# Performance work log

Measured on AMD Instinct MI355X. Metric: run time of the kernel, lower is better.

## Reference

```python
import jax, jax.numpy as jnp
import numpy as np

STALK_DIM = 16
N_NODES = 50000
N_EDGES = 400000
HIDDEN = 64


def setup_inputs() -> dict:
    key = jax.random.key(0)
    k1, k2, k3, k4 = jax.random.split(key, 4)
    d = STALK_DIM
    x = jax.random.normal(k1, (N_NODES, d), dtype=jnp.float32)
    edge_index = jax.random.randint(k2, (2, N_EDGES), 0, N_NODES, dtype=jnp.int64)
    W1 = jax.random.normal(k3, (HIDDEN, 2 * d), dtype=jnp.float32) * (1.0 / np.sqrt(2 * d))
    b1 = jnp.zeros((HIDDEN,), dtype=jnp.float32)
    W2 = jax.random.normal(k4, (d, HIDDEN), dtype=jnp.float32) * (1.0 / np.sqrt(HIDDEN))
    b2 = jnp.zeros((d,), dtype=jnp.float32)
    return {"x": x, "edge_index": edge_index, "W1": W1, "b1": b1, "W2": W2, "b2": b2}


def reference(x, edge_index, W1, b1, W2, b2):
    d = x.shape[1]
    n = x.shape[0]
    src, dst = edge_index[0], edge_index[1]
    xs, xd = x[src], x[dst]  # [E, d]

    def reflection(a, b):
        h = jax.nn.relu(jnp.concatenate([a, b], axis=1) @ W1.T + b1)
        return h @ W2.T + b2  # [E, d]

    def householder(v):
        # F.normalize(v, dim=1): v / max(||v||, 1e-12)
        vn = v / jnp.maximum(jnp.linalg.norm(v, axis=1, keepdims=True), 1e-12)
        return jnp.eye(d, dtype=v.dtype)[None] - 2.0 * vn[:, :, None] * vn[:, None, :]

    F_s = householder(reflection(xs, xd))  # [E, d, d]
    F_d = householder(reflection(xd, xs))  # [E, d, d]
    L_sd = -jnp.einsum('eki,ekj->eij', F_s, F_d)  # -F_s^T @ F_d, [E, d, d]

    # degrees: both endpoints of every edge contribute 1
    ones_e = jnp.ones(src.shape[0], dtype=x.dtype)
    deg = jnp.zeros(n, dtype=x.dtype).at[src].add(ones_e).at[dst].add(ones_e)
    deg_inv_sqrt = 1.0 / jnp.sqrt(jnp.maximum(deg, 1e-5))
    # D_inv_sqrt is scalar*I per node, so normalization is a scalar coefficient per edge
    coef = deg_inv_sqrt[src] * deg_inv_sqrt[dst]  # [E]

    # out[s] -= D^-1/2_s L D^-1/2_d x[d] ; out[d] -= D^-1/2_d L^T D^-1/2_s x[s]
    msg_s = coef[:, None] * jnp.einsum('eij,ej->ei', L_sd, xd)  # goes to src
    msg_d = coef[:, None] * jnp.einsum('eji,ej->ei', L_sd, xs)  # goes to dst

    out = x - jnp.zeros_like(x).at[src].add(msg_s) - jnp.zeros_like(x).at[dst].add(msg_d)
    return jax.nn.relu(out)
```

## Files before the change

kernel.cpp:

```cpp
#include <hip/hip_runtime.h>
#include <hip/hip_bf16.h>
#include <hip/hip_fp16.h>

#define N_NODES 50000
#define N_EDGES 400000
#define D 16
#define HID 64

#define SCAN_B 256
#define SCAN_G ((N_NODES + SCAN_B - 1) / SCAN_B)

typedef unsigned short ushort_t;
typedef _Float16 h16x2 __attribute__((ext_vector_type(2)));

#define CNT4_OFF  0
#define DEG_OFF   (4 * N_NODES)
#define OFF_OFF   (5 * N_NODES)
#define CUR_OFF   (6 * N_NODES + 1)
#define BS_OFF    (7 * N_NODES + 1)
#define MSG_OFF_I (((BS_OFF + SCAN_G) + 3) & ~3)
#define PREP_OFF  (MSG_OFF_I + 2 * N_EDGES * D)
#define PREP_DW   (32 * 52 + 16)
#define CSR_NEEDED_BYTES ((size_t)(PREP_OFF + PREP_DW) * 4 + 64)

#define FB_NDEG   (N_NODES)
#define FB_NACC   (N_NODES * D)
#define FB_FLAGS  (FB_NDEG + FB_NACC)

__device__ __forceinline__ float bf_bits(ushort_t us) {
    return __uint_as_float(((unsigned)us) << 16);
}
__device__ __forceinline__ float lo_bf(unsigned u) { return __uint_as_float(u << 16); }
__device__ __forceinline__ float hi_bf(unsigned u) { return __uint_as_float(u & 0xffff0000u); }
__device__ __forceinline__ ushort_t f2bf(float v) {
    unsigned u = __float_as_uint(v);
    unsigned r = (u + 0x7fffu + ((u >> 16) & 1u)) >> 16;
    return (ushort_t)r;
}
__device__ __forceinline__ float ld_f(const void* p, int idx, int f32) {
    return f32 ? ((const float*)p)[idx]
               : bf_bits(((const ushort_t*)p)[idx]);
}

__device__ __forceinline__ unsigned pack_h2(float a, float b) {
#if __has_builtin(__builtin_amdgcn_cvt_pkrtz)
    return __builtin_bit_cast(unsigned, __builtin_amdgcn_cvt_pkrtz(a, b));
#else
    h16x2 h;
    h.x = (_Float16)a;
    h.y = (_Float16)b;
    return __builtin_bit_cast(unsigned, h);
#endif
}

#if __has_builtin(__builtin_amdgcn_fdot2)
__device__ __forceinline__ float fdot2u(unsigned a, unsigned b, float c) {
    return __builtin_amdgcn_fdot2(__builtin_bit_cast(h16x2, a),
                                  __builtin_bit_cast(h16x2, b), c, false);
}
#else
__device__ __forceinline__ float fdot2u(unsigned a, unsigned b, float c) {
    h16x2 ha = __builtin_bit_cast(h16x2, a);
    h16x2 hb = __builtin_bit_cast(h16x2, b);
    return fmaf((float)ha.x, (float)hb.x, fmaf((float)ha.y, (float)hb.y, c));
}
#endif

__device__ __forceinline__ void load16(const void* __restrict__ p, long long base,
                                       int f32, float* o) {
    if (f32) {
        const float4* q = (const float4*)((const float*)p + base);
        float4 a = q[0], b = q[1], c = q[2], d = q[3];
        o[0]=a.x; o[1]=a.y; o[2]=a.z; o[3]=a.w;
        o[4]=b.x; o[5]=b.y; o[6]=b.z; o[7]=b.w;
        o[8]=c.x; o[9]=c.y; o[10]=c.z; o[11]=c.w;
        o[12]=d.x; o[13]=d.y; o[14]=d.z; o[15]=d.w;
    } else {
        const uint4* q = (const uint4*)((const ushort_t*)p + base);
        uint4 a = q[0], b = q[1];
        unsigned u[8] = {a.x, a.y, a.z, a.w, b.x, b.y, b.z, b.w};
#pragma unroll
        for (int k = 0; k < 8; k++) {
            o[2 * k]     = lo_bf(u[k]);
            o[2 * k + 1] = hi_bf(u[k]);
        }
    }
}

__device__ __forceinline__ void load_edge(const void* __restrict__ ei, int e, int is64,
                                          int& s, int& d) {
    if (is64) {
        const long long* p = (const long long*)ei;
        s = (int)p[e];
        d = (int)p[N_EDGES + e];
    } else {
        const int* p = (const int*)ei;
        s = p[e];
        d = p[N_EDGES + e];
    }
}

__device__ __forceinline__ void detect_flags(const void* x, const void* ei, int* flags) {
    const ushort_t* h = (const ushort_t*)x;
    int f32 = 0;
    for (int k = 0; k < 256; k++) {
        float v = bf_bits(h[k]);
        if (!(v == v) || fabsf(v) > 1.0e6f) { f32 = 1; break; }
    }
    const long long* p = (const long long*)ei;
    int i64 = 1;
    for (int k = 0; k < 16; k++) {
        long long v = p[k];
        if (v < 0 || v >= N_NODES) { i64 = 0; break; }
    }
    flags[0] = f32;
    flags[1] = i64;
}

__device__ __forceinline__ void stage_weights(
    const void* W1, const void* b1, const void* W2, const void* b2, int f32,
    float* sW1, float* sW2t, float* sb1, float* sb2)
{
    int t = threadIdx.x;
    for (int idx = t; idx < HID * 2 * D; idx += blockDim.x)
        sW1[idx] = ld_f(W1, idx, f32);
    for (int idx = t; idx < HID * D; idx += blockDim.x) {
        int j = idx / D, i = idx % D;
        sW2t[idx] = ld_f(W2, i * HID + j, f32);
    }
    if (t < HID) sb1[t] = ld_f(b1, t, f32);
    if (t < D)  sb2[t] = ld_f(b2, t, f32);
}

__device__ __forceinline__ void edge_math_v4(
    const float* __restrict__ sW1, const float* __restrict__ sW2t,
    const float* __restrict__ sb1, const float* __restrict__ sb2,
    const float* xs, const float* xd, float coef,
    float* ms, float* md)
{
    float vs[D], vd[D];
#pragma unroll
    for (int i = 0; i < D; i++) { vs[i] = sb2[i]; vd[i] = sb2[i]; }
#pragma unroll 4
    for (int j = 0; j < HID; j++) {
        float hs = sb1[j], hd = sb1[j];
        const float4* w4 = (const float4*)&sW1[j * 2 * D];
#pragma unroll
        for (int t = 0; t < 4; t++) {
            float4 wv = w4[t];
            int k = 4 * t;
            hs = fmaf(wv.x, xs[k],     hs); hd = fmaf(wv.x, xd[k],     hd);
            hs = fmaf(wv.y, xs[k + 1], hs); hd = fmaf(wv.y, xd[k + 1], hd);
            hs = fmaf(wv.z, xs[k + 2], hs); hd = fmaf(wv.z, xd[k + 2], hd);
            hs = fmaf(wv.w, xs[k + 3], hs); hd = fmaf(wv.w, xd[k + 3], hd);
        }
#pragma unroll
        for (int t = 0; t < 4; t++) {
            float4 wv = w4[4 + t];
            int k = 4 * t;
            hs = fmaf(wv.x, xd[k],     hs); hd = fmaf(wv.x, xs[k],     hd);
            hs = fmaf(wv.y, xd[k + 1], hs); hd = fmaf(wv.y, xs[k + 1], hd);
            hs = fmaf(wv.z, xd[k + 2], hs); hd = fmaf(wv.z, xs[k + 2], hd);
            hs = fmaf(wv.w, xd[k + 3], hs); hd = fmaf(wv.w, xs[k + 3], hd);
        }
        hs = fmaxf(hs, 0.0f);
        hd = fmaxf(hd, 0.0f);
        const float4* w24 = (const float4*)&sW2t[j * D];
#pragma unroll
        for (int t = 0; t < 4; t++) {
            float4 u = w24[t];
            int i = 4 * t;
            vs[i]     = fmaf(u.x, hs, vs[i]);     vd[i]     = fmaf(u.x, hd, vd[i]);
            vs[i + 1] = fmaf(u.y, hs, vs[i + 1]); vd[i + 1] = fmaf(u.y, hd, vd[i + 1]);
            vs[i + 2] = fmaf(u.z, hs, vs[i + 2]); vd[i + 2] = fmaf(u.z, hd, vd[i + 2]);
            vs[i + 3] = fmaf(u.w, hs, vs[i + 3]); vd[i + 3] = fmaf(u.w, hd, vd[i + 3]);
        }
    }
    float ns = 0.0f, nd = 0.0f;
#pragma unroll
    for (int i = 0; i < D; i++) { ns = fmaf(vs[i], vs[i], ns); nd = fmaf(vd[i], vd[i], nd); }
    float is_ = 1.0f / fmaxf(sqrtf(ns), 1e-12f);
    float id_ = 1.0f / fmaxf(sqrtf(nd), 1e-12f);
#pragma unroll
    for (int i = 0; i < D; i++) { vs[i] *= is_; vd[i] *= id_; }
    float dot1 = 0.0f;
#pragma unroll
    for (int i = 0; i < D; i++) dot1 = fmaf(vd[i], xd[i], dot1);
#pragma unroll
    for (int i = 0; i < D; i++) ms[i] = fmaf(-2.0f * dot1, vd[i], xd[i]);
    float dot2 = 0.0f;
#pragma unroll
    for (int i = 0; i < D; i++) dot2 = fmaf(vs[i], ms[i], dot2);
#pragma unroll
    for (int i = 0; i < D; i++) ms[i] = coef * fmaf(-2.0f * dot2, vs[i], ms[i]);
    float dot3 = 0.0f;
#pragma unroll
    for (int i = 0; i < D; i++) dot3 = fmaf(vs[i], xs[i], dot3);
#pragma unroll
    for (int i = 0; i < D; i++) md[i] = fmaf(-2.0f * dot3, vs[i], xs[i]);
    float dot4 = 0.0f;
#pragma unroll
    for (int i = 0; i < D; i++) dot4 = fmaf(vd[i], md[i], dot4);
#pragma unroll
    for (int i = 0; i < D; i++) md[i] = coef * fmaf(-2.0f * dot4, vd[i], md[i]);
}

__global__ void csr_count_kernel(const void* __restrict__ ei,
                                 const void* __restrict__ x,
                                 const void* __restrict__ W1,
                                 const void* __restrict__ b1,
                                 const void* __restrict__ W2,
                                 const void* __restrict__ b2,
                                 int* __restrict__ wsI) {
    __shared__ int sfl[2];
    if (threadIdx.x == 0) detect_flags(x, ei, sfl);
    __syncthreads();
    int i64 = sfl[1];

    if (blockIdx.x == 0) {
        unsigned* pp = (unsigned*)(wsI + PREP_OFF);
        const ushort_t* W1b = (const ushort_t*)W1;
        const ushort_t* W2b = (const ushort_t*)W2;
        const ushort_t* b1b = (const ushort_t*)b1;
        const ushort_t* b2b = (const ushort_t*)b2;
        for (int idx = threadIdx.x; idx < 32 * 52; idx += 256) {
            int jj = idx / 52, w = idx % 52;
            unsigned val = 0;
            if (w < 32) {
                int row = 2 * jj + (w >> 4), k2 = w & 15;
                val = pack_h2(bf_bits(W1b[row * 32 + 2 * k2]),
                              bf_bits(W1b[row * 32 + 2 * k2 + 1]));
            } else if (w < 48) {
                int i = w - 32;
                val = pack_h2(bf_bits(W2b[i * HID + 2 * jj]),
                              bf_bits(W2b[i * HID + 2 * jj + 1]));
            } else if (w == 48) {
                val = __float_as_uint(bf_bits(b1b[2 * jj]));
            } else if (w == 49) {
                val = __float_as_uint(bf_bits(b1b[2 * jj + 1]));
            }
            pp[idx] = val;
        }
        if (threadIdx.x < D)
            pp[32 * 52 + threadIdx.x] = __float_as_uint(bf_bits(b2b[threadIdx.x]));
    }

    int e = blockIdx.x * blockDim.x + threadIdx.x;
    if (e >= N_EDGES) return;
    int s, d;
    load_edge(ei, e, i64, s, d);
    int r = (e & 3) * N_NODES;
    atomicAdd(&wsI[CNT4_OFF + r + s], 1);
    atomicAdd(&wsI[CNT4_OFF + r + d], 1);
}

__global__ __launch_bounds__(SCAN_B) void csr_scan1_kernel(int* __restrict__ wsI) {
    __shared__ int sm[SCAN_B];
    int t = threadIdx.x;
    int g = blockIdx.x * SCAN_B + t;
    int c = 0;
    if (g < N_NODES) {
        c = wsI[CNT4_OFF + g] + wsI[CNT4_OFF + N_NODES + g]
          + wsI[CNT4_OFF + 2 * N_NODES + g] + wsI[CNT4_OFF + 3 * N_NODES + g];
        wsI[DEG_OFF + g] = c;
    }
    sm[t] = c;
    __syncthreads();
    for (int st = SCAN_B / 2; st > 0; st >>= 1) {
        if (t < st) sm[t] += sm[t + st];
        __syncthreads();
    }
    if (t == 0) wsI[BS_OFF + blockIdx.x] = sm[0];
}

__global__ __launch_bounds__(SCAN_B) void csr_scan3_kernel(int* __restrict__ wsI) {
    __shared__ int sB[SCAN_B];
    __shared__ int sm[SCAN_B];
    int t = threadIdx.x;
    int bsv = (t < SCAN_G) ? wsI[BS_OFF + t] : 0;
    sB[t] = bsv;
    __syncthreads();
    for (int st = 1; st < SCAN_B; st <<= 1) {
        int u = (t >= st) ? sB[t - st] : 0;
        __syncthreads();
        sB[t] += u;
        __syncthreads();
    }
    int blockBase = sB[blockIdx.x] - wsI[BS_OFF + blockIdx.x];

    int g = blockIdx.x * SCAN_B + t;
    int c = (g < N_NODES) ? wsI[DEG_OFF + g] : 0;
    sm[t] = c;
    __syncthreads();
    for (int st = 1; st < SCAN_B; st <<= 1) {
        int u = (t >= st) ? sm[t - st] : 0;
        __syncthreads();
        sm[t] += u;
        __syncthreads();
    }
    int excl = sm[t] - c + blockBase;
    if (g < N_NODES) {
        wsI[OFF_OFF + g] = excl;
        wsI[CUR_OFF + g] = excl;
        if (g == N_NODES - 1) wsI[OFF_OFF + N_NODES] = excl + c;
    }
}

__global__ __launch_bounds__(256) void csr_edge_kernel(
    const void* __restrict__ x,
    const void* __restrict__ ei,
    const void* __restrict__ W1,
    const void* __restrict__ b1,
    const void* __restrict__ W2,
    const void* __restrict__ b2,
    const unsigned* __restrict__ prep,
    int* __restrict__ wsI)
{
    __shared__ __align__(16) float sW1f[HID * 2 * D];
    __shared__ __align__(16) float sW2tf[HID * D];
    __shared__ float sb1[HID];
    __shared__ float sb2[D];
    __shared__ int sfl[2];

    if (threadIdx.x == 0) detect_flags(x, ei, sfl);
    __syncthreads();
    int f32 = sfl[0], i64 = sfl[1];
    int t = threadIdx.x;

    if (f32) {
        for (int idx = t; idx < HID * 2 * D; idx += 256)
            sW1f[idx] = ld_f(W1, idx, 1);
        for (int idx = t; idx < HID * D; idx += 256) {
            int j = idx / D, i = idx % D;
            sW2tf[idx] = ld_f(W2, i * HID + j, 1);
        }
        if (t < HID) sb1[t] = ld_f(b1, t, 1);
        if (t < D)  sb2[t] = ld_f(b2, t, 1);
        __syncthreads();
    }

    int e = blockIdx.x * 256 + t;
    if (e >= N_EDGES) return;

    int s, d;
    load_edge(ei, e, i64, s, d);
    float degs = (float)wsI[DEG_OFF + s];
    float degd = (float)wsI[DEG_OFF + d];
    float coef = (1.0f / sqrtf(fmaxf(degs, 1e-5f))) * (1.0f / sqrtf(fmaxf(degd, 1e-5f)));
    float* msg = (float*)(wsI + MSG_OFF_I);

    if (!f32) {
        unsigned xsh[8], xdh[8];
        {
            const uint4* q = (const uint4*)((const ushort_t*)x + (long long)s * D);
            uint4 a = q[0], b = q[1];
            unsigned u[8] = {a.x, a.y, a.z, a.w, b.x, b.y, b.z, b.w};
#pragma unroll
            for (int k = 0; k < 8; k++) xsh[k] = pack_h2(lo_bf(u[k]), hi_bf(u[k]));
        }
        {
            const uint4* q = (const uint4*)((const ushort_t*)x + (long long)d * D);
            uint4 a = q[0], b = q[1];
            unsigned u[8] = {a.x, a.y, a.z, a.w, b.x, b.y, b.z, b.w};
#pragma unroll
            for (int k = 0; k < 8; k++) xdh[k] = pack_h2(lo_bf(u[k]), hi_bf(u[k]));
        }

        const float* b2f = (const float*)(prep + 32 * 52);
        float vs[D], vd[D];
#pragma unroll
        for (int i = 0; i < D; i++) { vs[i] = b2f[i]; vd[i] = b2f[i]; }

#pragma unroll 1
        for (int jj = 0; jj < 32; jj++) {
            const uint4* wb = (const uint4*)(prep + jj * 52);
            uint4 q0 = wb[0], q1 = wb[1], q2 = wb[2], q3 = wb[3];
            uint4 q4 = wb[4], q5 = wb[5], q6 = wb[6], q7 = wb[7];
            uint4 q8 = wb[8], q9 = wb[9], qA = wb[10], qB = wb[11];
            const float* bb = (const float*)(prep + jj * 52 + 48);
            float hs0 = bb[0], hd0 = bb[0];
            float hs1 = bb[1], hd1 = bb[1];

            unsigned r0[16] = {q0.x, q0.y, q0.z, q0.w, q1.x, q1.y, q1.z, q1.w,
                               q2.x, q2.y, q2.z, q2.w, q3.x, q3.y, q3.z, q3.w};
            unsigned r1[16] = {q4.x, q4.y, q4.z, q4.w, q5.x, q5.y, q5.z, q5.w,
                               q6.x, q6.y, q6.z, q6.w, q7.x, q7.y, q7.z, q7.w};
            unsigned w2a[16] = {q8.x, q8.y, q8.z, q8.w, q9.x, q9.y, q9.z, q9.w,
                                qA.x, qA.y, qA.z, qA.w, qB.x, qB.y, qB.z, qB.w};
#pragma unroll
            for (int k = 0; k < 8; k++) {
                hs0 = fdot2u(r0[k], xsh[k], hs0);
                hd0 = fdot2u(r0[k], xdh[k], hd0);
                hs1 = fdot2u(r1[k], xsh[k], hs1);
                hd1 = fdot2u(r1[k], xdh[k], hd1);
            }
#pragma unroll
            for (int k = 0; k < 8; k++) {
                hs0 = fdot2u(r0[8 + k], xdh[k], hs0);
                hd0 = fdot2u(r0[8 + k], xsh[k], hd0);
                hs1 = fdot2u(r1[8 + k], xdh[k], hs1);
                hd1 = fdot2u(r1[8 + k], xsh[k], hd1);
            }
            hs0 = fmaxf(hs0, 0.0f); hd0 = fmaxf(hd0, 0.0f);
            hs1 = fmaxf(hs1, 0.0f); hd1 = fmaxf(hd1, 0.0f);
            unsigned hsp = pack_h2(hs0, hs1);
            unsigned hdp = pack_h2(hd0, hd1);
#pragma unroll
            for (int i = 0; i < D; i++) {
                vs[i] = fdot2u(w2a[i], hsp, vs[i]);
                vd[i] = fdot2u(w2a[i], hdp, vd[i]);
            }
        }

        float xs[D], xd[D];
#pragma unroll
        for (int k = 0; k < 8; k++) {
            h16x2 a = __builtin_bit_cast(h16x2, xsh[k]);
            xs[2 * k] = (float)a.x; xs[2 * k + 1] = (float)a.y;
            h16x2 b = __builtin_bit_cast(h16x2, xdh[k]);
            xd[2 * k] = (float)b.x; xd[2 * k + 1] = (float)b.y;
        }

        float ns = 0.0f, nd = 0.0f;
#pragma unroll
        for (int i = 0; i < D; i++) { ns = fmaf(vs[i], vs[i], ns); nd = fmaf(vd[i], vd[i], nd); }
        float is_ = 1.0f / fmaxf(sqrtf(ns), 1e-12f);
        float id_ = 1.0f / fmaxf(sqrtf(nd), 1e-12f);
#pragma unroll
        for (int i = 0; i < D; i++) { vs[i] *= is_; vd[i] *= id_; }

        float ms[D], md[D];
        float dot1 = 0.0f;
#pragma unroll
        for (int i = 0; i < D; i++) dot1 = fmaf(vd[i], xd[i], dot1);
#pragma unroll
        for (int i = 0; i < D; i++) ms[i] = fmaf(-2.0f * dot1, vd[i], xd[i]);
        float dot2 = 0.0f;
#pragma unroll
        for (int i = 0; i < D; i++) dot2 = fmaf(vs[i], ms[i], dot2);
#pragma unroll
        for (int i = 0; i < D; i++) ms[i] = coef * fmaf(-2.0f * dot2, vs[i], ms[i]);
        float dot3 = 0.0f;
#pragma unroll
        for (int i = 0; i < D; i++) dot3 = fmaf(vs[i], xs[i], dot3);
#pragma unroll
        for (int i = 0; i < D; i++) md[i] = fmaf(-2.0f * dot3, vs[i], xs[i]);
        float dot4 = 0.0f;
#pragma unroll
        for (int i = 0; i < D; i++) dot4 = fmaf(vd[i], md[i], dot4);
#pragma unroll
        for (int i = 0; i < D; i++) md[i] = coef * fmaf(-2.0f * dot4, vd[i], md[i]);

        int slot_s = atomicAdd(&wsI[CUR_OFF + s], 1);
        float4* m0 = (float4*)(msg + (long long)slot_s * D);
        m0[0] = make_float4(ms[0], ms[1], ms[2], ms[3]);
        m0[1] = make_float4(ms[4], ms[5], ms[6], ms[7]);
        m0[2] = make_float4(ms[8], ms[9], ms[10], ms[11]);
        m0[3] = make_float4(ms[12], ms[13], ms[14], ms[15]);
        int slot_d = atomicAdd(&wsI[CUR_OFF + d], 1);
        float4* m1 = (float4*)(msg + (long long)slot_d * D);
        m1[0] = make_float4(md[0], md[1], md[2], md[3]);
        m1[1] = make_float4(md[4], md[5], md[6], md[7]);
        m1[2] = make_float4(md[8], md[9], md[10], md[11]);
        m1[3] = make_float4(md[12], md[13], md[14], md[15]);
    } else {
        float xs[D], xd[D];
        load16(x, (long long)s * D, 1, xs);
        load16(x, (long long)d * D, 1, xd);
        float ms[D], md[D];
        edge_math_v4(sW1f, sW2tf, sb1, sb2, xs, xd, coef, ms, md);
        int slot_s = atomicAdd(&wsI[CUR_OFF + s], 1);
        float4* m0 = (float4*)(msg + (long long)slot_s * D);
        m0[0] = make_float4(ms[0], ms[1], ms[2], ms[3]);
        m0[1] = make_float4(ms[4], ms[5], ms[6], ms[7]);
        m0[2] = make_float4(ms[8], ms[9], ms[10], ms[11]);
        m0[3] = make_float4(ms[12], ms[13], ms[14], ms[15]);
        int slot_d = atomicAdd(&wsI[CUR_OFF + d], 1);
        float4* m1 = (float4*)(msg + (long long)slot_d * D);
        m1[0] = make_float4(md[0], md[1], md[2], md[3]);
        m1[1] = make_float4(md[4], md[5], md[6], md[7]);
        m1[2] = make_float4(md[8], md[9], md[10], md[11]);
        m1[3] = make_float4(md[12], md[13], md[14], md[15]);
    }
}

__global__ __launch_bounds__(256) void csr_gather_kernel(
    const void* __restrict__ x,
    const void* __restrict__ ei,
    const int* __restrict__ wsI,
    void* __restrict__ out)
{
    __shared__ int sfl[2];
    if (threadIdx.x == 0) detect_flags(x, ei, sfl);
    __syncthreads();
    int f32 = sfl[0];

    int n = blockIdx.x * 64 + (threadIdx.x >> 2);
    int c = threadIdx.x & 3;
    if (n >= N_NODES) return;

    const int* off = wsI + OFF_OFF;
    const float4* msg4 = (const float4*)(wsI + MSG_OFF_I);

    int beg = off[n], end = off[n + 1];
    float4 a = make_float4(0.0f, 0.0f, 0.0f, 0.0f);
    int it = beg;
    for (; it + 2 <= end; it += 2) {
        float4 u = msg4[(long long)it * 4 + c];
        float4 v = msg4[(long long)(it + 1) * 4 + c];
        a.x += u.x + v.x; a.y += u.y + v.y; a.z += u.z + v.z; a.w += u.w + v.w;
    }
    if (it < end) {
        float4 u = msg4[(long long)it * 4 + c];
        a.x += u.x; a.y += u.y; a.z += u.z; a.w += u.w;
    }

    long long xb = (long long)n * D + 4 * c;
    float4 xv;
    if (f32) {
        xv = *(const float4*)((const float*)x + xb);
    } else {
        uint2 u = *(const uint2*)((const ushort_t*)x + xb);
        xv.x = lo_bf(u.x); xv.y = hi_bf(u.x);
        xv.z = lo_bf(u.y); xv.w = hi_bf(u.y);
    }
    float4 r;
    r.x = fmaxf(xv.x + a.x, 0.0f);
    r.y = fmaxf(xv.y + a.y, 0.0f);
    r.z = fmaxf(xv.z + a.z, 0.0f);
    r.w = fmaxf(xv.w + a.w, 0.0f);
    if (f32) {
        *(float4*)((float*)out + xb) = r;
    } else {
        uint2 o;
        o.x = (unsigned)f2bf(r.x) | ((unsigned)f2bf(r.y) << 16);
        o.y = (unsigned)f2bf(r.z) | ((unsigned)f2bf(r.w) << 16);
        *(uint2*)((ushort_t*)out + xb) = o;
    }
}

__global__ void fb_init_kernel(float* __restrict__ ws,
                               const void* __restrict__ x,
                               const void* __restrict__ ei) {
    int i = blockIdx.x * blockDim.x + threadIdx.x;
    if (i < FB_FLAGS) ws[i] = 0.0f;
    if (blockIdx.x == 0 && threadIdx.x == 0)
        detect_flags(x, ei, (int*)(ws + FB_FLAGS));
}

__global__ void fb_deg_kernel(const void* __restrict__ ei, float* __restrict__ ws) {
    int i64 = ((const int*)(ws + FB_FLAGS))[1];
    int e = blockIdx.x * blockDim.x + threadIdx.x;
    if (e >= N_EDGES) return;
    int s, d;
    load_edge(ei, e, i64, s, d);
    atomicAdd(&ws[s], 1.0f);
    atomicAdd(&ws[d], 1.0f);
}

__global__ __launch_bounds__(256) void fb_edge_kernel(
    const void* __restrict__ x, const void* __restrict__ ei,
    const void* __restrict__ W1, const void* __restrict__ b1,
    const void* __restrict__ W2, const void* __restrict__ b2,
    float* __restrict__ ws)
{
    __shared__ __align__(16) float sW1[HID * 2 * D];
    __shared__ __align__(16) float sW2t[HID * D];
    __shared__ float sb1[HID];
    __shared__ float sb2[D];
    const int* flags = (const int*)(ws + FB_FLAGS);
    int f32 = flags[0], i64 = flags[1];
    stage_weights(W1, b1, W2, b2, f32, sW1, sW2t, sb1, sb2);
    __syncthreads();
    int e = blockIdx.x * blockDim.x + threadIdx.x;
    if (e >= N_EDGES) return;
    int s, d;
    load_edge(ei, e, i64, s, d);
    float xs[D], xd[D];
    load16(x, (long long)s * D, f32, xs);
    load16(x, (long long)d * D, f32, xd);
    float coef = (1.0f / sqrtf(fmaxf(ws[s], 1e-5f))) * (1.0f / sqrtf(fmaxf(ws[d], 1e-5f)));
    float ms[D], md[D];
    edge_math_v4(sW1, sW2t, sb1, sb2, xs, xd, coef, ms, md);
    float* acc = ws + FB_NDEG;
#pragma unroll
    for (int i = 0; i < D; i++) atomicAdd(&acc[(long long)s * D + i], ms[i]);
#pragma unroll
    for (int i = 0; i < D; i++) atomicAdd(&acc[(long long)d * D + i], md[i]);
}

__global__ void fb_finalize_kernel(const void* __restrict__ x,
                                   const float* __restrict__ ws,
                                   void* __restrict__ out)
{
    int f32 = ((const int*)(ws + FB_FLAGS))[0];
    const float* acc = ws + FB_NDEG;
    int i = blockIdx.x * blockDim.x + threadIdx.x;
    if (i >= FB_NACC) return;
    float v = ld_f(x, i, f32) + acc[i];
    v = fmaxf(v, 0.0f);
    if (f32) ((float*)out)[i] = v;
    else     ((__hip_bfloat16*)out)[i] = __float2bfloat16(v);
}

extern "C" void kernel_launch(void* const* d_in, const int* in_sizes, int n_in,
                              void* d_out, int out_size, void* d_ws, size_t ws_size,
                              hipStream_t stream)
{
    const void* x  = d_in[0];
    const void* ei = d_in[1];
    const void* W1 = d_in[2];
    const void* b1 = d_in[3];
    const void* W2 = d_in[4];
    const void* b2 = d_in[5];

    int blk = 256;
    if (ws_size >= CSR_NEEDED_BYTES) {
        int* wsI = (int*)d_ws;
        hipMemsetAsync(d_ws, 0, (size_t)4 * N_NODES * sizeof(int), stream);
        csr_count_kernel<<<(N_EDGES + blk - 1) / blk, blk, 0, stream>>>(ei, x, W1, b1, W2, b2, wsI);
        csr_scan1_kernel<<<SCAN_G, SCAN_B, 0, stream>>>(wsI);
        csr_scan3_kernel<<<SCAN_G, SCAN_B, 0, stream>>>(wsI);
        csr_edge_kernel<<<(N_EDGES + blk - 1) / blk, blk, 0, stream>>>(
            x, ei, W1, b1, W2, b2, (const unsigned*)(wsI + PREP_OFF), wsI);
        csr_gather_kernel<<<(N_NODES + 63) / 64, blk, 0, stream>>>(x, ei, wsI, d_out);
    } else {
        float* ws = (float*)d_ws;
        fb_init_kernel<<<(FB_FLAGS + blk - 1) / blk, blk, 0, stream>>>(ws, x, ei);
        fb_deg_kernel<<<(N_EDGES + blk - 1) / blk, blk, 0, stream>>>(ei, ws);
        fb_edge_kernel<<<(N_EDGES + blk - 1) / blk, blk, 0, stream>>>(x, ei, W1, b1, W2, b2, ws);
        fb_finalize_kernel<<<(FB_NACC + blk - 1) / blk, blk, 0, stream>>>(x, ws, d_out);
    }
}
```

Baseline: 205.9 us.

## Replace fp16 dot2 edge MLP with fp32 FMAs and parallelize input-format detection

The bf16 edge path stops packing inputs and weights into fp16 pairs for fdot2 and runs the MLP in fp32 FMAs over a 64x64 fp32 prepared weight table. The serial single-thread format detection in every block becomes a wavefront ballot over 64 threads. The goal is to cut the per-block serial flag-check latency and to improve accuracy. The trade-off is roughly double the ALU instructions and weight loads in the MLP inner loop.

```diff
diff --git a/kernel.cpp b/kernel.cpp
--- a/kernel.cpp
+++ b/kernel.cpp
@@ -11,7 +11,6 @@
 #define SCAN_G ((N_NODES + SCAN_B - 1) / SCAN_B)
 
 typedef unsigned short ushort_t;
-typedef _Float16 h16x2 __attribute__((ext_vector_type(2)));
 
 #define CNT4_OFF  0
 #define DEG_OFF   (4 * N_NODES)
@@ -20,7 +19,7 @@
 #define BS_OFF    (7 * N_NODES + 1)
 #define MSG_OFF_I (((BS_OFF + SCAN_G) + 3) & ~3)
 #define PREP_OFF  (MSG_OFF_I + 2 * N_EDGES * D)
-#define PREP_DW   (32 * 52 + 16)
+#define PREP_DW   (64 * 64 + 16)
 #define CSR_NEEDED_BYTES ((size_t)(PREP_OFF + PREP_DW) * 4 + 64)
 
 #define FB_NDEG   (N_NODES)
@@ -41,30 +40,6 @@
     return f32 ? ((const float*)p)[idx]
                : bf_bits(((const ushort_t*)p)[idx]);
 }
-
-__device__ __forceinline__ unsigned pack_h2(float a, float b) {
-#if __has_builtin(__builtin_amdgcn_cvt_pkrtz)
-    return __builtin_bit_cast(unsigned, __builtin_amdgcn_cvt_pkrtz(a, b));
-#else
-    h16x2 h;
-    h.x = (_Float16)a;
-    h.y = (_Float16)b;
-    return __builtin_bit_cast(unsigned, h);
-#endif
-}
-
-#if __has_builtin(__builtin_amdgcn_fdot2)
-__device__ __forceinline__ float fdot2u(unsigned a, unsigned b, float c) {
-    return __builtin_amdgcn_fdot2(__builtin_bit_cast(h16x2, a),
-                                  __builtin_bit_cast(h16x2, b), c, false);
-}
-#else
-__device__ __forceinline__ float fdot2u(unsigned a, unsigned b, float c) {
-    h16x2 ha = __builtin_bit_cast(h16x2, a);
-    h16x2 hb = __builtin_bit_cast(h16x2, b);
-    return fmaf((float)ha.x, (float)hb.x, fmaf((float)ha.y, (float)hb.y, c));
-}
-#endif
 
 __device__ __forceinline__ void load16(const void* __restrict__ p, long long base,
                                        int f32, float* o) {
@@ -100,21 +75,30 @@
     }
 }
 
-__device__ __forceinline__ void detect_flags(const void* x, const void* ei, int* flags) {
-    const ushort_t* h = (const ushort_t*)x;
-    int f32 = 0;
-    for (int k = 0; k < 256; k++) {
-        float v = bf_bits(h[k]);
-        if (!(v == v) || fabsf(v) > 1.0e6f) { f32 = 1; break; }
-    }
-    const long long* p = (const long long*)ei;
-    int i64 = 1;
-    for (int k = 0; k < 16; k++) {
-        long long v = p[k];
-        if (v < 0 || v >= N_NODES) { i64 = 0; break; }
-    }
-    flags[0] = f32;
-    flags[1] = i64;
+__device__ __forceinline__ void detect_flags_par(const void* x, const void* ei,
+                                                 int* flags) {
+    int t = threadIdx.x;
+    if (t < 64) {
+        const ushort_t* h = (const ushort_t*)x;
+        int bad = 0;
+#pragma unroll
+        for (int k = 0; k < 4; k++) {
+            float v = bf_bits(h[4 * t + k]);
+            if (!(v == v) || fabsf(v) > 1.0e6f) bad = 1;
+        }
+        unsigned long long mb = __ballot(bad);
+        const long long* p = (const long long*)ei;
+        int bad64 = 0;
+        if (t < 16) {
+            long long v = p[t];
+            bad64 = (v < 0 || v >= N_NODES) ? 1 : 0;
+        }
+        unsigned long long m64 = __ballot(bad64);
+        if (t == 0) {
+            flags[0] = mb ? 1 : 0;
+            flags[1] = m64 ? 0 : 1;
+        }
+    }
 }
 
 __device__ __forceinline__ void stage_weights(
@@ -213,36 +197,26 @@
                                  const void* __restrict__ b2,
                                  int* __restrict__ wsI) {
     __shared__ int sfl[2];
-    if (threadIdx.x == 0) detect_flags(x, ei, sfl);
+    detect_flags_par(x, ei, sfl);
     __syncthreads();
     int i64 = sfl[1];
 
     if (blockIdx.x == 0) {
-        unsigned* pp = (unsigned*)(wsI + PREP_OFF);
+        float* pf = (float*)(wsI + PREP_OFF);
         const ushort_t* W1b = (const ushort_t*)W1;
         const ushort_t* W2b = (const ushort_t*)W2;
         const ushort_t* b1b = (const ushort_t*)b1;
         const ushort_t* b2b = (const ushort_t*)b2;
-        for (int idx = threadIdx.x; idx < 32 * 52; idx += 256) {
-            int jj = idx / 52, w = idx % 52;
-            unsigned val = 0;
-            if (w < 32) {
-                int row = 2 * jj + (w >> 4), k2 = w & 15;
-                val = pack_h2(bf_bits(W1b[row * 32 + 2 * k2]),
-                              bf_bits(W1b[row * 32 + 2 * k2 + 1]));
-            } else if (w < 48) {
-                int i = w - 32;
-                val = pack_h2(bf_bits(W2b[i * HID + 2 * jj]),
-                              bf_bits(W2b[i * HID + 2 * jj + 1]));
-            } else if (w == 48) {
-                val = __float_as_uint(bf_bits(b1b[2 * jj]));
-            } else if (w == 49) {
-                val = __float_as_uint(bf_bits(b1b[2 * jj + 1]));
-            }
-            pp[idx] = val;
+        for (int idx = threadIdx.x; idx < 64 * 64; idx += 256) {
+            int j = idx >> 6, w = idx & 63;
+            float val = 0.0f;
+            if (w < 32)      val = bf_bits(W1b[j * 32 + w]);
+            else if (w < 48) val = bf_bits(W2b[(w - 32) * HID + j]);
+            else if (w == 48) val = bf_bits(b1b[j]);
+            pf[idx] = val;
         }
         if (threadIdx.x < D)
-            pp[32 * 52 + threadIdx.x] = __float_as_uint(bf_bits(b2b[threadIdx.x]));
+            pf[64 * 64 + threadIdx.x] = bf_bits(b2b[threadIdx.x]);
     }
 
     int e = blockIdx.x * blockDim.x + threadIdx.x;
@@ -313,7 +287,7 @@
     const void* __restrict__ b1,
     const void* __restrict__ W2,
     const void* __restrict__ b2,
-    const unsigned* __restrict__ prep,
+    const float* __restrict__ prep,
     int* __restrict__ wsI)
 {
     __shared__ __align__(16) float sW1f[HID * 2 * D];
@@ -322,7 +296,7 @@
     __shared__ float sb2[D];
     __shared__ int sfl[2];
 
-    if (threadIdx.x == 0) detect_flags(x, ei, sfl);
+    detect_flags_par(x, ei, sfl);
     __syncthreads();
     int f32 = sfl[0], i64 = sfl[1];
     int t = threadIdx.x;
@@ -349,76 +323,43 @@
     float coef = (1.0f / sqrtf(fmaxf(degs, 1e-5f))) * (1.0f / sqrtf(fmaxf(degd, 1e-5f)));
     float* msg = (float*)(wsI + MSG_OFF_I);
 
+    float xs[D], xd[D];
+    load16(x, (long long)s * D, f32, xs);
+    load16(x, (long long)d * D, f32, xd);
+
+    float ms[D], md[D];
     if (!f32) {
-        unsigned xsh[8], xdh[8];
-        {
-            const uint4* q = (const uint4*)((const ushort_t*)x + (long long)s * D);
-            uint4 a = q[0], b = q[1];
-            unsigned u[8] = {a.x, a.y, a.z, a.w, b.x, b.y, b.z, b.w};
-#pragma unroll
-            for (int k = 0; k < 8; k++) xsh[k] = pack_h2(lo_bf(u[k]), hi_bf(u[k]));
-        }
-        {
-            const uint4* q = (const uint4*)((const ushort_t*)x + (long long)d * D);
-            uint4 a = q[0], b = q[1];
-            unsigned u[8] = {a.x, a.y, a.z, a.w, b.x, b.y, b.z, b.w};
-#pragma unroll
-            for (int k = 0; k < 8; k++) xdh[k] = pack_h2(lo_bf(u[k]), hi_bf(u[k]));
-        }
-
-        const float* b2f = (const float*)(prep + 32 * 52);
+        const float* b2f = prep + 64 * 64;
         float vs[D], vd[D];
 #pragma unroll
         for (int i = 0; i < D; i++) { vs[i] = b2f[i]; vd[i] = b2f[i]; }
 
 #pragma unroll 1
-        for (int jj = 0; jj < 32; jj++) {
-            const uint4* wb = (const uint4*)(prep + jj * 52);
-            uint4 q0 = wb[0], q1 = wb[1], q2 = wb[2], q3 = wb[3];
-            uint4 q4 = wb[4], q5 = wb[5], q6 = wb[6], q7 = wb[7];
-            uint4 q8 = wb[8], q9 = wb[9], qA = wb[10], qB = wb[11];
-            const float* bb = (const float*)(prep + jj * 52 + 48);
-            float hs0 = bb[0], hd0 = bb[0];
-            float hs1 = bb[1], hd1 = bb[1];
-
-            unsigned r0[16] = {q0.x, q0.y, q0.z, q0.w, q1.x, q1.y, q1.z, q1.w,
-                               q2.x, q2.y, q2.z, q2.w, q3.x, q3.y, q3.z, q3.w};
-            unsigned r1[16] = {q4.x, q4.y, q4.z, q4.w, q5.x, q5.y, q5.z, q5.w,
-                               q6.x, q6.y, q6.z, q6.w, q7.x, q7.y, q7.z, q7.w};
-            unsigned w2a[16] = {q8.x, q8.y, q8.z, q8.w, q9.x, q9.y, q9.z, q9.w,
-                                qA.x, qA.y, qA.z, qA.w, qB.x, qB.y, qB.z, qB.w};
+        for (int j = 0; j < HID; j++) {
+            const float* w = prep + (j << 6);
+            float b1j = w[48];
+            float hs0 = b1j, hs1 = 0.0f, hd0 = b1j, hd1 = 0.0f;
 #pragma unroll
             for (int k = 0; k < 8; k++) {
-                hs0 = fdot2u(r0[k], xsh[k], hs0);
-                hd0 = fdot2u(r0[k], xdh[k], hd0);
-                hs1 = fdot2u(r1[k], xsh[k], hs1);
-                hd1 = fdot2u(r1[k], xdh[k], hd1);
+                hs0 = fmaf(w[k],     xs[k],     hs0);
+                hd0 = fmaf(w[k],     xd[k],     hd0);
+                hs1 = fmaf(w[8 + k], xs[8 + k], hs1);
+                hd1 = fmaf(w[8 + k], xd[8 + k], hd1);
             }
 #pragma unroll
             for (int k = 0; k < 8; k++) {
-                hs0 = fdot2u(r0[8 + k], xdh[k], hs0);
-                hd0 = fdot2u(r0[8 + k], xsh[k], hd0);
-                hs1 = fdot2u(r1[8 + k], xdh[k], hs1);
-                hd1 = fdot2u(r1[8 + k], xsh[k], hd1);
+                hs0 = fmaf(w[16 + k], xd[k],     hs0);
+                hd0 = fmaf(w[16 + k], xs[k],     hd0);
+                hs1 = fmaf(w[24 + k], xd[8 + k], hs1);
+                hd1 = fmaf(w[24 + k], xs[8 + k], hd1);
             }
-            hs0 = fmaxf(hs0, 0.0f); hd0 = fmaxf(hd0, 0.0f);
-            hs1 = fmaxf(hs1, 0.0f); hd1 = fmaxf(hd1, 0.0f);
-            unsigned hsp = pack_h2(hs0, hs1);
-            unsigned hdp = pack_h2(hd0, hd1);
+            float hs = fmaxf(hs0 + hs1, 0.0f);
+            float hd = fmaxf(hd0 + hd1, 0.0f);
 #pragma unroll
             for (int i = 0; i < D; i++) {
-                vs[i] = fdot2u(w2a[i], hsp, vs[i]);
-                vd[i] = fdot2u(w2a[i], hdp, vd[i]);
+                vs[i] = fmaf(w[32 + i], hs, vs[i]);
+                vd[i] = fmaf(w[32 + i], hd, vd[i]);
             }
-        }
-
-        float xs[D], xd[D];
-#pragma unroll
-        for (int k = 0; k < 8; k++) {
-            h16x2 a = __builtin_bit_cast(h16x2, xsh[k]);
-            xs[2 * k] = (float)a.x; xs[2 * k + 1] = (float)a.y;
-            h16x2 b = __builtin_bit_cast(h16x2, xdh[k]);
-            xd[2 * k] = (float)b.x; xd[2 * k + 1] = (float)b.y;
         }
 
         float ns = 0.0f, nd = 0.0f;
@@ -429,7 +370,6 @@
 #pragma unroll
         for (int i = 0; i < D; i++) { vs[i] *= is_; vd[i] *= id_; }
 
-        float ms[D], md[D];
         float dot1 = 0.0f;
 #pragma unroll
         for (int i = 0; i < D; i++) dot1 = fmaf(vd[i], xd[i], dot1);
@@ -450,38 +390,22 @@
         for (int i = 0; i < D; i++) dot4 = fmaf(vd[i], md[i], dot4);
 #pragma unroll
         for (int i = 0; i < D; i++) md[i] = coef * fmaf(-2.0f * dot4, vd[i], md[i]);
-
-        int slot_s = atomicAdd(&wsI[CUR_OFF + s], 1);
-        float4* m0 = (float4*)(msg + (long long)slot_s * D);
-        m0[0] = make_float4(ms[0], ms[1], ms[2], ms[3]);
-        m0[1] = make_float4(ms[4], ms[5], ms[6], ms[7]);
-        m0[2] = make_float4(ms[8], ms[9], ms[10], ms[11]);
-        m0[3] = make_float4(ms[12], ms[13], ms[14], ms[15]);
-        int slot_d = atomicAdd(&wsI[CUR_OFF + d], 1);
-        float4* m1 = (float4*)(msg + (long long)slot_d * D);
-        m1[0] = make_float4(md[0], md[1], md[2], md[3]);
-        m1[1] = make_float4(md[4], md[5], md[6], md[7]);
-        m1[2] = make_float4(md[8], md[9], md[10], md[11]);
-        m1[3] = make_float4(md[12], md[13], md[14], md[15]);
     } else {
-        float xs[D], xd[D];
-        load16(x, (long long)s * D, 1, xs);
-        load16(x, (long long)d * D, 1, xd);
-        float ms[D], md[D];
         edge_math_v4(sW1f, sW2tf, sb1, sb2, xs, xd, coef, ms, md);
-        int slot_s = atomicAdd(&wsI[CUR_OFF + s], 1);
-        float4* m0 = (float4*)(msg + (long long)slot_s * D);
-        m0[0] = make_float4(ms[0], ms[1], ms[2], ms[3]);
-        m0[1] = make_float4(ms[4], ms[5], ms[6], ms[7]);
-        m0[2] = make_float4(ms[8], ms[9], ms[10], ms[11]);
-        m0[3] = make_float4(ms[12], ms[13], ms[14], ms[15]);
-        int slot_d = atomicAdd(&wsI[CUR_OFF + d], 1);
-        float4* m1 = (float4*)(msg + (long long)slot_d * D);
-        m1[0] = make_float4(md[0], md[1], md[2], md[3]);
-        m1[1] = make_float4(md[4], md[5], md[6], md[7]);
-        m1[2] = make_float4(md[8], md[9], md[10], md[11]);
-        m1[3] = make_float4(md[12], md[13], md[14], md[15]);
-    }
+    }
+
+    int slot_s = atomicAdd(&wsI[CUR_OFF + s], 1);
+    float4* m0 = (float4*)(msg + (long long)slot_s * D);
+    m0[0] = make_float4(ms[0], ms[1], ms[2], ms[3]);
+    m0[1] = make_float4(ms[4], ms[5], ms[6], ms[7]);
+    m0[2] = make_float4(ms[8], ms[9], ms[10], ms[11]);
+    m0[3] = make_float4(ms[12], ms[13], ms[14], ms[15]);
+    int slot_d = atomicAdd(&wsI[CUR_OFF + d], 1);
+    float4* m1 = (float4*)(msg + (long long)slot_d * D);
+    m1[0] = make_float4(md[0], md[1], md[2], md[3]);
+    m1[1] = make_float4(md[4], md[5], md[6], md[7]);
+    m1[2] = make_float4(md[8], md[9], md[10], md[11]);
+    m1[3] = make_float4(md[12], md[13], md[14], md[15]);
 }
 
 __global__ __launch_bounds__(256) void csr_gather_kernel(
@@ -491,7 +415,7 @@
     void* __restrict__ out)
 {
     __shared__ int sfl[2];
-    if (threadIdx.x == 0) detect_flags(x, ei, sfl);
+    detect_flags_par(x, ei, sfl);
     __syncthreads();
     int f32 = sfl[0];
 
@@ -544,8 +468,8 @@
                                const void* __restrict__ ei) {
     int i = blockIdx.x * blockDim.x + threadIdx.x;
     if (i < FB_FLAGS) ws[i] = 0.0f;
-    if (blockIdx.x == 0 && threadIdx.x == 0)
-        detect_flags(x, ei, (int*)(ws + FB_FLAGS));
+    if (blockIdx.x == 0)
+        detect_flags_par(x, ei, (int*)(ws + FB_FLAGS));
 }
 
 __global__ void fb_deg_kernel(const void* __restrict__ ei, float* __restrict__ ws) {
@@ -622,7 +546,7 @@
         csr_scan1_kernel<<<SCAN_G, SCAN_B, 0, stream>>>(wsI);
         csr_scan3_kernel<<<SCAN_G, SCAN_B, 0, stream>>>(wsI);
         csr_edge_kernel<<<(N_EDGES + blk - 1) / blk, blk, 0, stream>>>(
-            x, ei, W1, b1, W2, b2, (const unsigned*)(wsI + PREP_OFF), wsI);
+            x, ei, W1, b1, W2, b2, (const float*)(wsI + PREP_OFF), wsI);
         csr_gather_kernel<<<(N_NODES + 63) / 64, blk, 0, stream>>>(x, ei, wsI, d_out);
     } else {
         float* ws = (float*)d_ws;
```

After: 204.7 us. About the same (-0.6%).
